# Optimization experiments

Hardware: AMD Instinct MI355X
Metric: run time of the kernel (lower is better)

The kernel has to match this reference:

```python
import jax, jax.numpy as jnp
import numpy as np

N, C, D, H = 4096, 64, 128, 4
CD = 2 * D          # combined_dim = 2*input_size
DQ = CD // 8        # per-head query/key dim


def _mlp(x, W1, b1, W2, b2):
    # MLP(in, hidden, out): Linear -> ReLU -> Linear
    return jax.nn.relu(x @ W1.T + b1) @ W2.T + b2


def _gru(x, h, Wih, bih, Whh, bhh):
    # torch.nn.GRUCell math
    gi = x @ Wih.T + bih
    gh = h @ Whh.T + bhh
    ir, iz, inn = jnp.split(gi, 3, axis=-1)
    hr, hz, hn = jnp.split(gh, 3, axis=-1)
    r = jax.nn.sigmoid(ir + hr)
    z = jax.nn.sigmoid(iz + hz)
    n = jnp.tanh(inn + r * hn)
    return (1.0 - z) * n + z * h


def setup_inputs() -> dict:
    key = jax.random.key(0)
    ks = jax.random.split(key, 16)
    def w(k, shape, fan):
        return jax.random.normal(k, shape, jnp.float32) / np.float32(np.sqrt(fan))
    return {
        "x": jax.random.normal(ks[0], (N, D), jnp.float32),
        "h": jax.random.normal(ks[1], (N, D), jnp.float32),
        "cluster_h": jax.random.normal(ks[2], (C, D), jnp.float32),
        "query_vectors": jax.random.normal(ks[3], (C, D), jnp.float32),
        "cluster_labels": jax.random.randint(ks[4], (N,), 0, C),
        "nodes_ind": jnp.arange(N),
        "edge_index_intra": jax.random.randint(ks[5], (2, 1024), 0, N),
        "num_clusters": C,
        "Wq": w(ks[6], (H, DQ, CD), CD), "bq": jnp.zeros((H, DQ), jnp.float32),
        "Wk": w(ks[7], (H, DQ, CD), CD), "bk": jnp.zeros((H, DQ), jnp.float32),
        "Wv": w(ks[8], (H, CD, CD), CD), "bv": jnp.zeros((H, CD), jnp.float32),
        "W1": w(ks[9], (CD, H * CD), H * CD), "b1": jnp.zeros((CD,), jnp.float32),
        "W2": w(ks[10], (CD, CD), CD), "b2": jnp.zeros((CD,), jnp.float32),
        "gru_Wih": w(ks[11], (3 * D, D), D), "gru_bih": jnp.zeros((3 * D,), jnp.float32),
        "gru_Whh": w(ks[12], (3 * D, D), D), "gru_bhh": jnp.zeros((3 * D,), jnp.float32),
        "Wp": 0.1 * w(ks[13], (D, D), D), "bp": jnp.zeros((D,), jnp.float32),
    }


def reference(x, h, cluster_h, query_vectors, cluster_labels, nodes_ind,
              edge_index_intra, num_clusters,
              Wq, bq, Wk, bk, Wv, bv, W1, b1, W2, b2,
              gru_Wih, gru_bih, gru_Whh, gru_bhh, Wp, bp):
    combined = jnp.concatenate([x, h], axis=-1)              # [N, 2D]
    # multi-head dense attention over all nodes (heads vectorized)
    q = jnp.einsum('nd,hed->hne', combined, Wq) + bq[:, None, :]   # [H,N,DQ]
    k = jnp.einsum('nd,hed->hne', combined, Wk) + bk[:, None, :]
    v = jnp.einsum('nd,hed->hne', combined, Wv) + bv[:, None, :]   # [H,N,2D]
    scores = jnp.einsum('hne,hme->hnm', q, k) / jnp.sqrt(jnp.float32(DQ))
    attn = jax.nn.softmax(jax.nn.leaky_relu(scores, 0.2), axis=-1)  # [H,N,N]
    hp = jnp.einsum('hnm,hme->hne', attn, v)                 # [H,N,2D]
    hp = jnp.transpose(hp, (1, 0, 2)).reshape(combined.shape[0], -1)  # [N,H*2D]
    node_repr = _mlp(hp, W1, b1, W2, b2) + combined          # [N,2D]
    # per-cluster mean of previous node hidden states
    ones = jnp.ones((h.shape[0],), h.dtype)
    counts = jax.ops.segment_sum(ones, cluster_labels, num_segments=num_clusters)
    sums = jax.ops.segment_sum(h, cluster_labels, num_segments=num_clusters)
    agg = sums / jnp.maximum(counts, 1.0)[:, None]           # [C,D]
    present = (counts > 0)[:, None]
    new_ch = _gru(agg, cluster_h, gru_Wih, gru_bih, gru_Whh, gru_bhh)
    updated_cluster_h = jnp.where(present, new_ch, cluster_h)  # [C,D]
    # cluster-to-node projection broadcast back to nodes
    c2n = (updated_cluster_h @ Wp.T + bp)[cluster_labels]    # [N,D]
    updated_h = node_repr[:, D:] + c2n                       # [N,D]
    return updated_h, updated_cluster_h
```

## Files before the change

### kernel.cpp

```cpp
#include <hip/hip_runtime.h>
#include <math.h>

#define N_NODES 4096
#define NHEADS  4
#define NSPLIT  4
#define KVRANGE 1024

typedef _Float16 f16;
typedef _Float16 half8 __attribute__((ext_vector_type(8)));
typedef float f32x4 __attribute__((ext_vector_type(4)));

template <int EPI>
__device__ __forceinline__ void gemm_body(const f16* __restrict__ A,
                                          const f16* __restrict__ B,
                                          const float* __restrict__ bias,
                                          const float* __restrict__ resid,
                                          const int* __restrict__ lab,
                                          const float* __restrict__ c2n,
                                          void* __restrict__ outv,
                                          int M, int K, int J, float alpha,
                                          int bx, int by, f16* smem) {
  f16* As = smem;
  f16* Bs = smem + 64 * 64;
  const int t  = threadIdx.x;
  const int mb = bx * 64, jb = by * 64;
  const int w  = t >> 6, l = t & 63;
  const int g_ = l >> 4, c_ = l & 15;
  const int m0 = (w >> 1) * 32, n0 = (w & 1) * 32;

  f32x4 acc[2][2];
#pragma unroll
  for (int i = 0; i < 2; ++i)
#pragma unroll
    for (int j = 0; j < 2; ++j) acc[i][j] = (f32x4){0.f, 0.f, 0.f, 0.f};

#define FRAG16(BUF, row, kh) \
  (*(const half8*)&BUF[(size_t)(row) * 64 + (((((kh) * 4 + g_) ^ (c_ & 7))) << 3)])

  for (int kb = 0; kb < K; kb += 64) {
    __syncthreads();
#pragma unroll
    for (int i = 0; i < 2; ++i) {
      int f = t + i * 256;
      int r = f >> 3, ch = f & 7;
      *(uint4*)&As[r * 64 + ((ch ^ (r & 7)) << 3)] =
          *(const uint4*)&A[(size_t)(mb + r) * K + kb + ch * 8];
      *(uint4*)&Bs[r * 64 + ((ch ^ (r & 7)) << 3)] =
          *(const uint4*)&B[(size_t)(jb + r) * K + kb + ch * 8];
    }
    __syncthreads();
#pragma unroll
    for (int kh = 0; kh < 2; ++kh) {
      half8 a0 = FRAG16(As, m0 + c_, kh);
      half8 a1 = FRAG16(As, m0 + 16 + c_, kh);
      half8 b0 = FRAG16(Bs, n0 + c_, kh);
      half8 b1 = FRAG16(Bs, n0 + 16 + c_, kh);
      acc[0][0] = __builtin_amdgcn_mfma_f32_16x16x32_f16(a0, b0, acc[0][0], 0, 0, 0);
      acc[0][1] = __builtin_amdgcn_mfma_f32_16x16x32_f16(a0, b1, acc[0][1], 0, 0, 0);
      acc[1][0] = __builtin_amdgcn_mfma_f32_16x16x32_f16(a1, b0, acc[1][0], 0, 0, 0);
      acc[1][1] = __builtin_amdgcn_mfma_f32_16x16x32_f16(a1, b1, acc[1][1], 0, 0, 0);
    }
  }
#undef FRAG16

#pragma unroll
  for (int mt = 0; mt < 2; ++mt)
#pragma unroll
    for (int nt = 0; nt < 2; ++nt) {
      int mbase = mb + m0 + mt * 16 + g_ * 4;
      int jj    = jb + n0 + nt * 16 + c_;
      if (EPI == 0 || EPI == 1) {
        f16* out = (f16*)outv;
        float bc = bias[jj];
#pragma unroll
        for (int r = 0; r < 4; ++r) {
          float v = (acc[mt][nt][r] + bc) * alpha;
          if (EPI == 1) v = fmaxf(v, 0.f);
          out[(size_t)(mbase + r) * J + jj] = (f16)v;
        }
      } else if (EPI == 2) {
        f16* out = (f16*)outv;
#pragma unroll
        for (int r = 0; r < 4; ++r)
          out[(size_t)(mbase + r) * J + jj] = (f16)(acc[mt][nt][r] + bias[mbase + r]);
      } else {
        float* out = (float*)outv;
        float bc = bias[jj];
#pragma unroll
        for (int r = 0; r < 4; ++r) {
          int m = mbase + r;
          out[(size_t)m * J + jj] = acc[mt][nt][r] + bc +
              resid[(size_t)m * J + jj] + c2n[lab[m] * 128 + jj];
        }
      }
    }
}

template <int EPI>
__global__ __launch_bounds__(256) void k_gemm16(const f16* __restrict__ A,
                                                const f16* __restrict__ B,
                                                const float* __restrict__ bias,
                                                const float* __restrict__ resid,
                                                const int* __restrict__ lab,
                                                const float* __restrict__ c2n,
                                                void* __restrict__ outv,
                                                int M, int K, int J, float alpha) {
  __shared__ f16 smem[2 * 64 * 64];
  gemm_body<EPI>(A, B, bias, resid, lab, c2n, outv, M, K, J, alpha,
                 blockIdx.x, blockIdx.y, smem);
}

__global__ __launch_bounds__(256) void k_prep(const float* __restrict__ x,
                                              const float* __restrict__ h,
                                              const float* __restrict__ Wq,
                                              const float* __restrict__ Wk,
                                              const float* __restrict__ Wv,
                                              const float* __restrict__ W1,
                                              const float* __restrict__ W2,
                                              f16* __restrict__ comb16,
                                              f16* __restrict__ pool,
                                              float* __restrict__ sums) {
  const int b = blockIdx.x, t = threadIdx.x;
  if (b < 1024) {
    int i = b * 256 + t;
    int n = i >> 6, c = i & 63;
    float4 v;
    if (c < 32) v = ((const float4*)x)[n * 32 + c];
    else        v = ((const float4*)h)[n * 32 + (c - 32)];
    union { uint2 u; f16 h4[4]; } pk;
    pk.h4[0] = (f16)v.x; pk.h4[1] = (f16)v.y; pk.h4[2] = (f16)v.z; pk.h4[3] = (f16)v.w;
    *(uint2*)&comb16[(size_t)i * 4] = pk.u;
  } else if (b < 1664) {
    int i4 = ((b - 1024) * 256 + t) * 4;
    const float* src; int off;
    if      (i4 <  32768) { src = Wq; off = 0; }
    else if (i4 <  65536) { src = Wk; off = 32768; }
    else if (i4 < 327680) { src = Wv; off = 65536; }
    else if (i4 < 589824) { src = W1; off = 327680; }
    else                  { src = W2; off = 589824; }
    float4 v = *(const float4*)&src[i4 - off];
    union { uint2 u; f16 h4[4]; } pk;
    pk.h4[0] = (f16)v.x; pk.h4[1] = (f16)v.y; pk.h4[2] = (f16)v.z; pk.h4[3] = (f16)v.w;
    *(uint2*)&pool[i4] = pk.u;
  } else {
    int i = (b - 1664) * 256 + t;
    if (i < 8256) sums[i] = 0.f;
  }
}

__global__ __launch_bounds__(256) void k_qkv(const f16* __restrict__ comb16,
                                             const f16* __restrict__ wq16,
                                             const f16* __restrict__ wk16,
                                             const f16* __restrict__ wv16,
                                             const float* __restrict__ bq,
                                             const float* __restrict__ bk,
                                             const float* __restrict__ bv,
                                             f16* __restrict__ qf16,
                                             f16* __restrict__ kf16,
                                             f16* __restrict__ vt16,
                                             const float* __restrict__ h,
                                             const int* __restrict__ lab,
                                             float* __restrict__ sums,
                                             float* __restrict__ cnt,
                                             float qscale) {
  __shared__ f16 smem[2 * 64 * 64];
  const int b = blockIdx.x;
  if (b < 1024) {
    gemm_body<2>(wv16, comb16, bv, nullptr, nullptr, nullptr, vt16,
                 1024, 256, 4096, 1.0f, b & 15, b >> 4, smem);
  } else if (b < 1152) {
    int r = b - 1024;
    gemm_body<0>(comb16, wq16, bq, nullptr, nullptr, nullptr, qf16,
                 4096, 256, 128, qscale, r & 63, r >> 6, smem);
  } else if (b < 1280) {
    int r = b - 1152;
    gemm_body<0>(comb16, wk16, bk, nullptr, nullptr, nullptr, kf16,
                 4096, 256, 128, 1.0f, r & 63, r >> 6, smem);
  } else {
    int i = (b - 1280) * 256 + threadIdx.x;
    int n = i >> 7, d = i & 127;
    int c = lab[n];
    atomicAdd(&sums[c * 128 + d], h[i]);
    if (d == 0) atomicAdd(&cnt[c], 1.0f);
  }
}

__global__ __launch_bounds__(256, 3) void k_attn_mfma(const f16* __restrict__ qg,
                                                      const f16* __restrict__ kg,
                                                      const f16* __restrict__ vt,
                                                      f16* __restrict__ pO,
                                                      float* __restrict__ pM,
                                                      float* __restrict__ pL) {
  const int hd  = blockIdx.y;
  const int sp  = blockIdx.z;
  const int kv0 = sp * KVRANGE;
  const int t   = threadIdx.x;
  const int w   = t >> 6, l = t & 63;
  const int g   = l >> 4, c = l & 15;
  const int qb  = blockIdx.x * 64;

  __shared__ f16 Ks[32 * 40];
  __shared__ f16 Vs[256 * 40];
  __shared__ f16 Ps[64 * 40];
  __shared__ float CfS[64];

  half8 qf = *(const half8*)&qg[(size_t)(qb + w * 16 + c) * 128 + hd * 32 + g * 8];

  f32x4 oacc[4][4];
#pragma unroll
  for (int i = 0; i < 4; ++i)
#pragma unroll
    for (int j = 0; j < 4; ++j) oacc[i][j] = (f32x4){0.f, 0.f, 0.f, 0.f};
  float m_run = -INFINITY, l_run = 0.f;
  const f32x4 zero4 = {0.f, 0.f, 0.f, 0.f};

  for (int kb = 0; kb < KVRANGE; kb += 32) {
    __syncthreads();
    if (t < 128) {
      int r = t >> 2, c8 = (t & 3) * 8;
      *(uint4*)&Ks[r * 40 + c8] =
          *(const uint4*)&kg[(size_t)(kv0 + kb + r) * 128 + hd * 32 + c8];
    }
#pragma unroll
    for (int i = 0; i < 4; ++i) {
      int cc = i * 256 + t, d = cc >> 2, c8 = (cc & 3) * 8;
      *(uint4*)&Vs[d * 40 + c8] =
          *(const uint4*)&vt[(size_t)(hd * 256 + d) * 4096 + kv0 + kb + c8];
    }
    __syncthreads();

    f32x4 s0 = __builtin_amdgcn_mfma_f32_16x16x32_f16(
        *(const half8*)&Ks[(c) * 40 + g * 8], qf, zero4, 0, 0, 0);
    f32x4 s1 = __builtin_amdgcn_mfma_f32_16x16x32_f16(
        *(const half8*)&Ks[(16 + c) * 40 + g * 8], qf, zero4, 0, 0, 0);

    float sv[8];
#pragma unroll
    for (int r = 0; r < 4; ++r) {
      float a = s0[r]; sv[r]     = a > 0.f ? a : 0.2f * a;
      float b = s1[r]; sv[4 + r] = b > 0.f ? b : 0.2f * b;
    }
    float mx = sv[0];
#pragma unroll
    for (int r = 1; r < 8; ++r) mx = fmaxf(mx, sv[r]);
    mx = fmaxf(mx, __shfl_xor(mx, 16));
    mx = fmaxf(mx, __shfl_xor(mx, 32));

    float cf = 1.f;
    if (!__all(mx <= m_run + 8.f)) {
      float m_new = fmaxf(m_run, mx);
      cf = __expf(m_run - m_new);
      m_run = m_new;
    }
    float p[8], ps = 0.f;
#pragma unroll
    for (int r = 0; r < 8; ++r) { p[r] = __expf(sv[r] - m_run); ps += p[r]; }
    ps += __shfl_xor(ps, 16);
    ps += __shfl_xor(ps, 32);
    l_run = l_run * cf + ps;

    if (g == 0) CfS[w * 16 + c] = cf;
    {
      union { unsigned u; f16 h2[2]; } z;
      uint2 lo, hi;
      z.h2[0] = (f16)p[0]; z.h2[1] = (f16)p[1]; lo.x = z.u;
      z.h2[0] = (f16)p[2]; z.h2[1] = (f16)p[3]; lo.y = z.u;
      z.h2[0] = (f16)p[4]; z.h2[1] = (f16)p[5]; hi.x = z.u;
      z.h2[0] = (f16)p[6]; z.h2[1] = (f16)p[7]; hi.y = z.u;
      *(uint2*)&Ps[(w * 16 + c) * 40 + g * 4]      = lo;
      *(uint2*)&Ps[(w * 16 + c) * 40 + 16 + g * 4] = hi;
    }
    __syncthreads();

#pragma unroll
    for (int qt = 0; qt < 4; ++qt) {
      float cfq = CfS[qt * 16 + c];
      if (!__all(cfq == 1.f)) {
#pragma unroll
        for (int i = 0; i < 4; ++i) {
          oacc[i][qt][0] *= cfq; oacc[i][qt][1] *= cfq;
          oacc[i][qt][2] *= cfq; oacc[i][qt][3] *= cfq;
        }
      }
    }
    half8 pfr[4];
#pragma unroll
    for (int qt = 0; qt < 4; ++qt)
      pfr[qt] = *(const half8*)&Ps[(qt * 16 + c) * 40 + g * 8];
#pragma unroll
    for (int i = 0; i < 4; ++i) {
      half8 vfr = *(const half8*)&Vs[((w * 4 + i) * 16 + c) * 40 + g * 8];
#pragma unroll
      for (int qt = 0; qt < 4; ++qt)
        oacc[i][qt] = __builtin_amdgcn_mfma_f32_16x16x32_f16(vfr, pfr[qt], oacc[i][qt], 0, 0, 0);
    }
  }

  __syncthreads();
  if (g == 0) CfS[w * 16 + c] = l_run;
  __syncthreads();
  float linv[4];
#pragma unroll
  for (int qt = 0; qt < 4; ++qt) linv[qt] = 1.f / CfS[qt * 16 + c];
#pragma unroll
  for (int i = 0; i < 4; ++i)
#pragma unroll
    for (int qt = 0; qt < 4; ++qt)
#pragma unroll
      for (int r = 0; r < 4; ++r) {
        int j = hd * 256 + (w * 4 + i) * 16 + g * 4 + r;
        pO[(size_t)(sp * 1024 + j) * 4096 + qb + qt * 16 + c] =
            (f16)(oacc[i][qt][r] * linv[qt]);
      }
  if (g == 0) {
    pM[(sp * 4 + hd) * 4096 + qb + w * 16 + c] = m_run;
    pL[(sp * 4 + hd) * 4096 + qb + w * 16 + c] = l_run;
  }
}

__global__ __launch_bounds__(256) void k_mergeplus(const f16* __restrict__ pO,
                                                   const float* __restrict__ pM,
                                                   const float* __restrict__ pL,
                                                   f16* __restrict__ hp,
                                                   const float* __restrict__ sums,
                                                   const float* __restrict__ cnt,
                                                   const float* __restrict__ ch,
                                                   const float* __restrict__ gWih,
                                                   const float* __restrict__ gbih,
                                                   const float* __restrict__ gWhh,
                                                   const float* __restrict__ gbhh,
                                                   const float* __restrict__ Wp,
                                                   const float* __restrict__ bp,
                                                   float* __restrict__ out_uch,
                                                   float* __restrict__ c2n) {
  const int b = blockIdx.x, t = threadIdx.x;
  if (b < 1024) {
    __shared__ float wm[NSPLIT][64], wl[NSPLIT][64];
    __shared__ float tile[64][65];
    const int q0 = (b & 63) * 64, jb = (b >> 6) * 64;
    const int h  = jb >> 8;

    if (t < 64) {
#pragma unroll
      for (int s = 0; s < NSPLIT; ++s) {
        wm[s][t] = pM[(s * 4 + h) * 4096 + q0 + t];
        wl[s][t] = pL[(s * 4 + h) * 4096 + q0 + t];
      }
    }
    __syncthreads();

    const int q8 = (t & 7) * 8;
#pragma unroll
    for (int it = 0; it < 2; ++it) {
      int jl = (t >> 3) + it * 32;
      float wgt[NSPLIT][8], inv[8];
#pragma unroll
      for (int q = 0; q < 8; ++q) {
        float M = wm[0][q8 + q];
#pragma unroll
        for (int s = 1; s < NSPLIT; ++s) M = fmaxf(M, wm[s][q8 + q]);
        float den = 0.f;
#pragma unroll
        for (int s = 0; s < NSPLIT; ++s) {
          float wv = wl[s][q8 + q] * __expf(wm[s][q8 + q] - M);
          wgt[s][q] = wv; den += wv;
        }
        inv[q] = 1.f / den;
      }
      float o[8] = {0.f};
#pragma unroll
      for (int s = 0; s < NSPLIT; ++s) {
        union { uint4 u; f16 h8[8]; } raw;
        raw.u = *(const uint4*)&pO[(size_t)(s * 1024 + jb + jl) * 4096 + q0 + q8];
#pragma unroll
        for (int q = 0; q < 8; ++q) o[q] += wgt[s][q] * (float)raw.h8[q];
      }
#pragma unroll
      for (int q = 0; q < 8; ++q) tile[q8 + q][jl] = o[q] * inv[q];
    }
    __syncthreads();

#pragma unroll
    for (int it = 0; it < 2; ++it) {
      int ql = (t >> 3) + it * 32, chk = t & 7;
      union { uint4 u; f16 h8[8]; } pk;
#pragma unroll
      for (int k = 0; k < 8; ++k) pk.h8[k] = (f16)tile[ql][chk * 8 + k];
      *(uint4*)&hp[(size_t)(q0 + ql) * 1024 + jb + chk * 8] = pk.u;
    }
  } else {
    __shared__ float ax[2][128], hx[2][128], ul[2][128];
    const int cc = t >> 7, d = t & 127;
    const int c  = (b - 1024) * 2 + cc;
    float count = cnt[c];
    ax[cc][d] = sums[c * 128 + d] / fmaxf(count, 1.0f);
    hx[cc][d] = ch[c * 128 + d];
    __syncthreads();
    float gi[3], gh[3];
#pragma unroll
    for (int g = 0; g < 3; ++g) {
      const float4* wi4 = (const float4*)&gWih[(size_t)(g * 128 + d) * 128];
      const float4* wh4 = (const float4*)&gWhh[(size_t)(g * 128 + d) * 128];
      float si = 0.f, sh = 0.f;
#pragma unroll 8
      for (int e = 0; e < 32; ++e) {
        float4 wv = wi4[e], hv = wh4[e];
        si = fmaf(ax[cc][e*4+0], wv.x, si); si = fmaf(ax[cc][e*4+1], wv.y, si);
        si = fmaf(ax[cc][e*4+2], wv.z, si); si = fmaf(ax[cc][e*4+3], wv.w, si);
        sh = fmaf(hx[cc][e*4+0], hv.x, sh); sh = fmaf(hx[cc][e*4+1], hv.y, sh);
        sh = fmaf(hx[cc][e*4+2], hv.z, sh); sh = fmaf(hx[cc][e*4+3], hv.w, sh);
      }
      gi[g] = si + gbih[g * 128 + d];
      gh[g] = sh + gbhh[g * 128 + d];
    }
    float r = 1.f / (1.f + expf(-(gi[0] + gh[0])));
    float z = 1.f / (1.f + expf(-(gi[1] + gh[1])));
    float nn = tanhf(gi[2] + r * gh[2]);
    float hv = hx[cc][d];
    float nh = (1.f - z) * nn + z * hv;
    float res = (count > 0.f) ? nh : hv;
    ul[cc][d] = res;
    out_uch[c * 128 + d] = res;
    __syncthreads();
    const float4* w4 = (const float4*)&Wp[(size_t)d * 128];
    float s = 0.f;
#pragma unroll 8
    for (int e = 0; e < 32; ++e) {
      float4 wv = w4[e];
      s = fmaf(ul[cc][e*4+0], wv.x, s); s = fmaf(ul[cc][e*4+1], wv.y, s);
      s = fmaf(ul[cc][e*4+2], wv.z, s); s = fmaf(ul[cc][e*4+3], wv.w, s);
    }
    c2n[c * 128 + d] = s + bp[d];
  }
}

extern "C" void kernel_launch(void* const* d_in, const int* in_sizes, int n_in,
                              void* d_out, int out_size, void* d_ws, size_t ws_size,
                              hipStream_t stream) {
  const float* x    = (const float*)d_in[0];
  const float* h    = (const float*)d_in[1];
  const float* ch   = (const float*)d_in[2];
  const int*   lab  = (const int*)d_in[4];
  const float* Wq   = (const float*)d_in[8];
  const float* bq   = (const float*)d_in[9];
  const float* Wk   = (const float*)d_in[10];
  const float* bk   = (const float*)d_in[11];
  const float* Wv   = (const float*)d_in[12];
  const float* bv   = (const float*)d_in[13];
  const float* W1   = (const float*)d_in[14];
  const float* b1   = (const float*)d_in[15];
  const float* W2   = (const float*)d_in[16];
  const float* b2   = (const float*)d_in[17];
  const float* gWih = (const float*)d_in[18];
  const float* gbih = (const float*)d_in[19];
  const float* gWhh = (const float*)d_in[20];
  const float* gbhh = (const float*)d_in[21];
  const float* Wp   = (const float*)d_in[22];
  const float* bp   = (const float*)d_in[23];

  float* outp    = (float*)d_out;
  float* out_uch = outp + 4096 * 128;

  f16* comb16 = (f16*)d_ws;
  f16* w16    = comb16 + 4096 * 256;
  f16* wq16   = w16;
  f16* wk16   = w16 + 32768;
  f16* wv16   = w16 + 65536;
  f16* w116   = w16 + 327680;
  f16* w216   = w16 + 589824;
  f16* qf16   = w16 + 655360;
  f16* kf16   = qf16 + 4096 * 128;
  f16* vt16   = kf16 + 4096 * 128;
  f16* pO     = vt16 + 1024 * 4096;
  f16* hp16   = pO + (size_t)NSPLIT * 1024 * 4096;
  f16* y116   = hp16 + (size_t)4096 * 1024;
  float* pM   = (float*)(y116 + 4096 * 256);
  float* pL   = pM + NSPLIT * 4 * 4096;
  float* sums = pL + NSPLIT * 4 * 4096;
  float* cnt  = sums + 64 * 128;
  float* c2n  = cnt + 64;

  const float qscale = 0.17677669529663687f;

  k_prep<<<1697, 256, 0, stream>>>(x, h, Wq, Wk, Wv, W1, W2, comb16, w16, sums);
  k_qkv<<<3328, 256, 0, stream>>>(comb16, wq16, wk16, wv16, bq, bk, bv,
                                  qf16, kf16, vt16, h, lab, sums, cnt, qscale);
  k_attn_mfma<<<dim3(64, NHEADS, NSPLIT), 256, 0, stream>>>(qf16, kf16, vt16, pO, pM, pL);
  k_mergeplus<<<1056, 256, 0, stream>>>(pO, pM, pL, hp16, sums, cnt, ch,
                                        gWih, gbih, gWhh, gbhh, Wp, bp, out_uch, c2n);
  k_gemm16<1><<<dim3(64, 4), 256, 0, stream>>>(hp16, w116, b1, nullptr, nullptr, nullptr,
                                               y116, 4096, 1024, 256, 1.0f);
  k_gemm16<3><<<dim3(64, 2), 256, 0, stream>>>(y116, w216 + 128 * 256, b2 + 128, h, lab, c2n,
                                               outp, 4096, 256, 128, 1.0f);
}
```

Measured before the change: 259.5 us.

## Load K/V fragments directly from global and remap attention blocks per XCD

The attention kernel stops staging K and V tiles through shared memory and instead has each lane load its MFMA fragments straight from global memory, which removes one barrier and the LDS round trip per KV step. The grid is flattened to 1D and remapped so that blocks sharing the same head/split land on the same XCD, improving L2 reuse of K/V. It also raises the occupancy hint to 4 blocks per CU and wraps the PV MFMA loop in s_setprio. The risk is redundant global loads, since every wave fetches the same K fragments and there are uncoalesced strided V reads.

```diff
diff --git a/kernel.cpp b/kernel.cpp
--- a/kernel.cpp
+++ b/kernel.cpp
@@ -185,26 +185,32 @@
   }
 }
 
-__global__ __launch_bounds__(256, 3) void k_attn_mfma(const f16* __restrict__ qg,
+__global__ __launch_bounds__(256, 4) void k_attn_mfma(const f16* __restrict__ qg,
                                                       const f16* __restrict__ kg,
                                                       const f16* __restrict__ vt,
                                                       f16* __restrict__ pO,
                                                       float* __restrict__ pM,
                                                       float* __restrict__ pL) {
-  const int hd  = blockIdx.y;
-  const int sp  = blockIdx.z;
-  const int kv0 = sp * KVRANGE;
-  const int t   = threadIdx.x;
-  const int w   = t >> 6, l = t & 63;
-  const int g   = l >> 4, c = l & 15;
-  const int qb  = blockIdx.x * 64;
-
-  __shared__ f16 Ks[32 * 40];
-  __shared__ f16 Vs[256 * 40];
+  const int b     = blockIdx.x;
+  const int xcd   = b & 7;
+  const int i_    = b >> 3;
+  const int combo = xcd * 2 + (i_ >> 6);
+  const int qblk  = i_ & 63;
+  const int hd    = combo >> 2, sp = combo & 3;
+  const int kv0   = sp * KVRANGE;
+  const int qb    = qblk * 64;
+
+  const int t = threadIdx.x;
+  const int w = t >> 6, l = t & 63;
+  const int g = l >> 4, c = l & 15;
+
   __shared__ f16 Ps[64 * 40];
   __shared__ float CfS[64];
 
   half8 qf = *(const half8*)&qg[(size_t)(qb + w * 16 + c) * 128 + hd * 32 + g * 8];
+
+  const f16* kbase = &kg[(size_t)(kv0)*128 + hd * 32 + g * 8];
+  const f16* vbase = &vt[(size_t)(hd * 256) * 4096 + kv0 + g * 8];
 
   f32x4 oacc[4][4];
 #pragma unroll
@@ -216,29 +222,22 @@
 
   for (int kb = 0; kb < KVRANGE; kb += 32) {
     __syncthreads();
-    if (t < 128) {
-      int r = t >> 2, c8 = (t & 3) * 8;
-      *(uint4*)&Ks[r * 40 + c8] =
-          *(const uint4*)&kg[(size_t)(kv0 + kb + r) * 128 + hd * 32 + c8];
-    }
-#pragma unroll
-    for (int i = 0; i < 4; ++i) {
-      int cc = i * 256 + t, d = cc >> 2, c8 = (cc & 3) * 8;
-      *(uint4*)&Vs[d * 40 + c8] =
-          *(const uint4*)&vt[(size_t)(hd * 256 + d) * 4096 + kv0 + kb + c8];
-    }
-    __syncthreads();
-
-    f32x4 s0 = __builtin_amdgcn_mfma_f32_16x16x32_f16(
-        *(const half8*)&Ks[(c) * 40 + g * 8], qf, zero4, 0, 0, 0);
-    f32x4 s1 = __builtin_amdgcn_mfma_f32_16x16x32_f16(
-        *(const half8*)&Ks[(16 + c) * 40 + g * 8], qf, zero4, 0, 0, 0);
+
+    half8 kf0 = *(const half8*)&kbase[(size_t)(kb + c) * 128];
+    half8 kf1 = *(const half8*)&kbase[(size_t)(kb + 16 + c) * 128];
+    half8 vfr[4];
+#pragma unroll
+    for (int i = 0; i < 4; ++i)
+      vfr[i] = *(const half8*)&vbase[(size_t)((w * 4 + i) * 16 + c) * 4096 + kb];
+
+    f32x4 s0 = __builtin_amdgcn_mfma_f32_16x16x32_f16(kf0, qf, zero4, 0, 0, 0);
+    f32x4 s1 = __builtin_amdgcn_mfma_f32_16x16x32_f16(kf1, qf, zero4, 0, 0, 0);
 
     float sv[8];
 #pragma unroll
     for (int r = 0; r < 4; ++r) {
       float a = s0[r]; sv[r]     = a > 0.f ? a : 0.2f * a;
-      float b = s1[r]; sv[4 + r] = b > 0.f ? b : 0.2f * b;
+      float b2 = s1[r]; sv[4 + r] = b2 > 0.f ? b2 : 0.2f * b2;
     }
     float mx = sv[0];
 #pragma unroll
@@ -287,13 +286,14 @@
 #pragma unroll
     for (int qt = 0; qt < 4; ++qt)
       pfr[qt] = *(const half8*)&Ps[(qt * 16 + c) * 40 + g * 8];
+    __builtin_amdgcn_s_setprio(1);
 #pragma unroll
     for (int i = 0; i < 4; ++i) {
-      half8 vfr = *(const half8*)&Vs[((w * 4 + i) * 16 + c) * 40 + g * 8];
 #pragma unroll
       for (int qt = 0; qt < 4; ++qt)
-        oacc[i][qt] = __builtin_amdgcn_mfma_f32_16x16x32_f16(vfr, pfr[qt], oacc[i][qt], 0, 0, 0);
-    }
+        oacc[i][qt] = __builtin_amdgcn_mfma_f32_16x16x32_f16(vfr[i], pfr[qt], oacc[i][qt], 0, 0, 0);
+    }
+    __builtin_amdgcn_s_setprio(0);
   }
 
   __syncthreads();
@@ -485,7 +485,7 @@
   k_prep<<<1697, 256, 0, stream>>>(x, h, Wq, Wk, Wv, W1, W2, comb16, w16, sums);
   k_qkv<<<3328, 256, 0, stream>>>(comb16, wq16, wk16, wv16, bq, bk, bv,
                                   qf16, kf16, vt16, h, lab, sums, cnt, qscale);
-  k_attn_mfma<<<dim3(64, NHEADS, NSPLIT), 256, 0, stream>>>(qf16, kf16, vt16, pO, pM, pL);
+  k_attn_mfma<<<1024, 256, 0, stream>>>(qf16, kf16, vt16, pO, pM, pL);
   k_mergeplus<<<1056, 256, 0, stream>>>(pO, pM, pL, hp16, sums, cnt, ch,
                                         gWih, gbih, gWhh, gbhh, Wp, bp, out_uch, c2n);
   k_gemm16<1><<<dim3(64, 4), 256, 0, stream>>>(hp16, w116, b1, nullptr, nullptr, nullptr,
```

Result: slower. 281.3 us (+8.4%).

## Prefetch GEMM tiles into registers and move cluster GRU into attention kernel

Applied to the files above, without the earlier changes.

The GEMM body now loads the next K-tile of A and B into registers after the barrier, so global loads overlap the MFMA work on the current shared-memory tile. The per-cluster GRU and projection work moves out of the merge kernel into 32 extra blocks of the attention grid, so it runs alongside the long attention blocks instead of sitting at the tail of the merge. This adds register pressure in the GEMM and shares LDS between two roles in the attention kernel.

```diff
diff --git a/kernel.cpp b/kernel.cpp
--- a/kernel.cpp
+++ b/kernel.cpp
@@ -27,28 +27,36 @@
   const int w  = t >> 6, l = t & 63;
   const int g_ = l >> 4, c_ = l & 15;
   const int m0 = (w >> 1) * 32, n0 = (w & 1) * 32;
+  const int r0 = t >> 3, ch0 = t & 7;
 
   f32x4 acc[2][2];
 #pragma unroll
   for (int i = 0; i < 2; ++i)
 #pragma unroll
     for (int j = 0; j < 2; ++j) acc[i][j] = (f32x4){0.f, 0.f, 0.f, 0.f};
+
+  uint4 ra0 = *(const uint4*)&A[(size_t)(mb + r0) * K + ch0 * 8];
+  uint4 ra1 = *(const uint4*)&A[(size_t)(mb + r0 + 32) * K + ch0 * 8];
+  uint4 rb0 = *(const uint4*)&B[(size_t)(jb + r0) * K + ch0 * 8];
+  uint4 rb1 = *(const uint4*)&B[(size_t)(jb + r0 + 32) * K + ch0 * 8];
+  const int sw = (ch0 ^ (r0 & 7)) << 3;
 
 #define FRAG16(BUF, row, kh) \
   (*(const half8*)&BUF[(size_t)(row) * 64 + (((((kh) * 4 + g_) ^ (c_ & 7))) << 3)])
 
   for (int kb = 0; kb < K; kb += 64) {
     __syncthreads();
-#pragma unroll
-    for (int i = 0; i < 2; ++i) {
-      int f = t + i * 256;
-      int r = f >> 3, ch = f & 7;
-      *(uint4*)&As[r * 64 + ((ch ^ (r & 7)) << 3)] =
-          *(const uint4*)&A[(size_t)(mb + r) * K + kb + ch * 8];
-      *(uint4*)&Bs[r * 64 + ((ch ^ (r & 7)) << 3)] =
-          *(const uint4*)&B[(size_t)(jb + r) * K + kb + ch * 8];
-    }
-    __syncthreads();
+    *(uint4*)&As[r0 * 64 + sw]        = ra0;
+    *(uint4*)&As[(r0 + 32) * 64 + sw] = ra1;
+    *(uint4*)&Bs[r0 * 64 + sw]        = rb0;
+    *(uint4*)&Bs[(r0 + 32) * 64 + sw] = rb1;
+    __syncthreads();
+    if (kb + 64 < K) {
+      ra0 = *(const uint4*)&A[(size_t)(mb + r0) * K + kb + 64 + ch0 * 8];
+      ra1 = *(const uint4*)&A[(size_t)(mb + r0 + 32) * K + kb + 64 + ch0 * 8];
+      rb0 = *(const uint4*)&B[(size_t)(jb + r0) * K + kb + 64 + ch0 * 8];
+      rb1 = *(const uint4*)&B[(size_t)(jb + r0 + 32) * K + kb + 64 + ch0 * 8];
+    }
 #pragma unroll
     for (int kh = 0; kh < 2; ++kh) {
       half8 a0 = FRAG16(As, m0 + c_, kh);
@@ -190,19 +198,80 @@
                                                       const f16* __restrict__ vt,
                                                       f16* __restrict__ pO,
                                                       float* __restrict__ pM,
-                                                      float* __restrict__ pL) {
-  const int hd  = blockIdx.y;
-  const int sp  = blockIdx.z;
-  const int kv0 = sp * KVRANGE;
-  const int t   = threadIdx.x;
-  const int w   = t >> 6, l = t & 63;
-  const int g   = l >> 4, c = l & 15;
-  const int qb  = blockIdx.x * 64;
-
+                                                      float* __restrict__ pL,
+                                                      const float* __restrict__ sums,
+                                                      const float* __restrict__ cnt,
+                                                      const float* __restrict__ ch,
+                                                      const float* __restrict__ gWih,
+                                                      const float* __restrict__ gbih,
+                                                      const float* __restrict__ gWhh,
+                                                      const float* __restrict__ gbhh,
+                                                      const float* __restrict__ Wp,
+                                                      const float* __restrict__ bp,
+                                                      float* __restrict__ out_uch,
+                                                      float* __restrict__ c2n) {
   __shared__ f16 Ks[32 * 40];
   __shared__ f16 Vs[256 * 40];
   __shared__ f16 Ps[64 * 40];
   __shared__ float CfS[64];
+
+  const int hd  = blockIdx.y;
+  const int sp  = blockIdx.z;
+  const int t   = threadIdx.x;
+
+  if (blockIdx.x >= 64) {
+    const int gid = (blockIdx.x - 64) * 16 + hd * 4 + sp;
+    float* ax = (float*)Vs;
+    float* hx = ax + 256;
+    float* ul = hx + 256;
+    const int cc = t >> 7, d = t & 127;
+    const int c  = gid * 2 + cc;
+    float count = cnt[c];
+    ax[cc * 128 + d] = sums[c * 128 + d] / fmaxf(count, 1.0f);
+    hx[cc * 128 + d] = ch[c * 128 + d];
+    __syncthreads();
+    float gi[3], gh[3];
+#pragma unroll
+    for (int g = 0; g < 3; ++g) {
+      const float4* wi4 = (const float4*)&gWih[(size_t)(g * 128 + d) * 128];
+      const float4* wh4 = (const float4*)&gWhh[(size_t)(g * 128 + d) * 128];
+      float si = 0.f, sh = 0.f;
+#pragma unroll 8
+      for (int e = 0; e < 32; ++e) {
+        float4 wv = wi4[e], hv = wh4[e];
+        si = fmaf(ax[cc*128+e*4+0], wv.x, si); si = fmaf(ax[cc*128+e*4+1], wv.y, si);
+        si = fmaf(ax[cc*128+e*4+2], wv.z, si); si = fmaf(ax[cc*128+e*4+3], wv.w, si);
+        sh = fmaf(hx[cc*128+e*4+0], hv.x, sh); sh = fmaf(hx[cc*128+e*4+1], hv.y, sh);
+        sh = fmaf(hx[cc*128+e*4+2], hv.z, sh); sh = fmaf(hx[cc*128+e*4+3], hv.w, sh);
+      }
+      gi[g] = si + gbih[g * 128 + d];
+      gh[g] = sh + gbhh[g * 128 + d];
+    }
+    float r = 1.f / (1.f + expf(-(gi[0] + gh[0])));
+    float z = 1.f / (1.f + expf(-(gi[1] + gh[1])));
+    float nn = tanhf(gi[2] + r * gh[2]);
+    float hv = hx[cc * 128 + d];
+    float nh = (1.f - z) * nn + z * hv;
+    float res = (count > 0.f) ? nh : hv;
+    ul[cc * 128 + d] = res;
+    out_uch[c * 128 + d] = res;
+    __syncthreads();
+    const float4* w4 = (const float4*)&Wp[(size_t)d * 128];
+    float s = 0.f;
+#pragma unroll 8
+    for (int e = 0; e < 32; ++e) {
+      float4 wv = w4[e];
+      s = fmaf(ul[cc*128+e*4+0], wv.x, s); s = fmaf(ul[cc*128+e*4+1], wv.y, s);
+      s = fmaf(ul[cc*128+e*4+2], wv.z, s); s = fmaf(ul[cc*128+e*4+3], wv.w, s);
+    }
+    c2n[c * 128 + d] = s + bp[d];
+    return;
+  }
+
+  const int kv0 = sp * KVRANGE;
+  const int w   = t >> 6, l = t & 63;
+  const int g   = l >> 4, c = l & 15;
+  const int qb  = blockIdx.x * 64;
 
   half8 qf = *(const half8*)&qg[(size_t)(qb + w * 16 + c) * 128 + hd * 32 + g * 8];
 
@@ -318,119 +387,63 @@
   }
 }
 
-__global__ __launch_bounds__(256) void k_mergeplus(const f16* __restrict__ pO,
-                                                   const float* __restrict__ pM,
-                                                   const float* __restrict__ pL,
-                                                   f16* __restrict__ hp,
-                                                   const float* __restrict__ sums,
-                                                   const float* __restrict__ cnt,
-                                                   const float* __restrict__ ch,
-                                                   const float* __restrict__ gWih,
-                                                   const float* __restrict__ gbih,
-                                                   const float* __restrict__ gWhh,
-                                                   const float* __restrict__ gbhh,
-                                                   const float* __restrict__ Wp,
-                                                   const float* __restrict__ bp,
-                                                   float* __restrict__ out_uch,
-                                                   float* __restrict__ c2n) {
+__global__ __launch_bounds__(256) void k_merge(const f16* __restrict__ pO,
+                                               const float* __restrict__ pM,
+                                               const float* __restrict__ pL,
+                                               f16* __restrict__ hp) {
   const int b = blockIdx.x, t = threadIdx.x;
-  if (b < 1024) {
-    __shared__ float wm[NSPLIT][64], wl[NSPLIT][64];
-    __shared__ float tile[64][65];
-    const int q0 = (b & 63) * 64, jb = (b >> 6) * 64;
-    const int h  = jb >> 8;
-
-    if (t < 64) {
+  __shared__ float wm[NSPLIT][64], wl[NSPLIT][64];
+  __shared__ float tile[64][65];
+  const int q0 = (b & 63) * 64, jb = (b >> 6) * 64;
+  const int h  = jb >> 8;
+
+  if (t < 64) {
+#pragma unroll
+    for (int s = 0; s < NSPLIT; ++s) {
+      wm[s][t] = pM[(s * 4 + h) * 4096 + q0 + t];
+      wl[s][t] = pL[(s * 4 + h) * 4096 + q0 + t];
+    }
+  }
+  __syncthreads();
+
+  const int q8 = (t & 7) * 8;
+#pragma unroll
+  for (int it = 0; it < 2; ++it) {
+    int jl = (t >> 3) + it * 32;
+    float wgt[NSPLIT][8], inv[8];
+#pragma unroll
+    for (int q = 0; q < 8; ++q) {
+      float M = wm[0][q8 + q];
+#pragma unroll
+      for (int s = 1; s < NSPLIT; ++s) M = fmaxf(M, wm[s][q8 + q]);
+      float den = 0.f;
 #pragma unroll
       for (int s = 0; s < NSPLIT; ++s) {
-        wm[s][t] = pM[(s * 4 + h) * 4096 + q0 + t];
-        wl[s][t] = pL[(s * 4 + h) * 4096 + q0 + t];
+        float wv = wl[s][q8 + q] * __expf(wm[s][q8 + q] - M);
+        wgt[s][q] = wv; den += wv;
       }
-    }
-    __syncthreads();
-
-    const int q8 = (t & 7) * 8;
-#pragma unroll
-    for (int it = 0; it < 2; ++it) {
-      int jl = (t >> 3) + it * 32;
-      float wgt[NSPLIT][8], inv[8];
-#pragma unroll
-      for (int q = 0; q < 8; ++q) {
-        float M = wm[0][q8 + q];
-#pragma unroll
-        for (int s = 1; s < NSPLIT; ++s) M = fmaxf(M, wm[s][q8 + q]);
-        float den = 0.f;
-#pragma unroll
-        for (int s = 0; s < NSPLIT; ++s) {
-          float wv = wl[s][q8 + q] * __expf(wm[s][q8 + q] - M);
-          wgt[s][q] = wv; den += wv;
-        }
-        inv[q] = 1.f / den;
-      }
-      float o[8] = {0.f};
-#pragma unroll
-      for (int s = 0; s < NSPLIT; ++s) {
-        union { uint4 u; f16 h8[8]; } raw;
-        raw.u = *(const uint4*)&pO[(size_t)(s * 1024 + jb + jl) * 4096 + q0 + q8];
-#pragma unroll
-        for (int q = 0; q < 8; ++q) o[q] += wgt[s][q] * (float)raw.h8[q];
-      }
-#pragma unroll
-      for (int q = 0; q < 8; ++q) tile[q8 + q][jl] = o[q] * inv[q];
-    }
-    __syncthreads();
-
-#pragma unroll
-    for (int it = 0; it < 2; ++it) {
-      int ql = (t >> 3) + it * 32, chk = t & 7;
-      union { uint4 u; f16 h8[8]; } pk;
-#pragma unroll
-      for (int k = 0; k < 8; ++k) pk.h8[k] = (f16)tile[ql][chk * 8 + k];
-      *(uint4*)&hp[(size_t)(q0 + ql) * 1024 + jb + chk * 8] = pk.u;
-    }
-  } else {
-    __shared__ float ax[2][128], hx[2][128], ul[2][128];
-    const int cc = t >> 7, d = t & 127;
-    const int c  = (b - 1024) * 2 + cc;
-    float count = cnt[c];
-    ax[cc][d] = sums[c * 128 + d] / fmaxf(count, 1.0f);
-    hx[cc][d] = ch[c * 128 + d];
-    __syncthreads();
-    float gi[3], gh[3];
-#pragma unroll
-    for (int g = 0; g < 3; ++g) {
-      const float4* wi4 = (const float4*)&gWih[(size_t)(g * 128 + d) * 128];
-      const float4* wh4 = (const float4*)&gWhh[(size_t)(g * 128 + d) * 128];
-      float si = 0.f, sh = 0.f;
-#pragma unroll 8
-      for (int e = 0; e < 32; ++e) {
-        float4 wv = wi4[e], hv = wh4[e];
-        si = fmaf(ax[cc][e*4+0], wv.x, si); si = fmaf(ax[cc][e*4+1], wv.y, si);
-        si = fmaf(ax[cc][e*4+2], wv.z, si); si = fmaf(ax[cc][e*4+3], wv.w, si);
-        sh = fmaf(hx[cc][e*4+0], hv.x, sh); sh = fmaf(hx[cc][e*4+1], hv.y, sh);
-        sh = fmaf(hx[cc][e*4+2], hv.z, sh); sh = fmaf(hx[cc][e*4+3], hv.w, sh);
-      }
-      gi[g] = si + gbih[g * 128 + d];
-      gh[g] = sh + gbhh[g * 128 + d];
-    }
-    float r = 1.f / (1.f + expf(-(gi[0] + gh[0])));
-    float z = 1.f / (1.f + expf(-(gi[1] + gh[1])));
-    float nn = tanhf(gi[2] + r * gh[2]);
-    float hv = hx[cc][d];
-    float nh = (1.f - z) * nn + z * hv;
-    float res = (count > 0.f) ? nh : hv;
-    ul[cc][d] = res;
-    out_uch[c * 128 + d] = res;
-    __syncthreads();
-    const float4* w4 = (const float4*)&Wp[(size_t)d * 128];
-    float s = 0.f;
-#pragma unroll 8
-    for (int e = 0; e < 32; ++e) {
-      float4 wv = w4[e];
-      s = fmaf(ul[cc][e*4+0], wv.x, s); s = fmaf(ul[cc][e*4+1], wv.y, s);
-      s = fmaf(ul[cc][e*4+2], wv.z, s); s = fmaf(ul[cc][e*4+3], wv.w, s);
-    }
-    c2n[c * 128 + d] = s + bp[d];
+      inv[q] = 1.f / den;
+    }
+    float o[8] = {0.f};
+#pragma unroll
+    for (int s = 0; s < NSPLIT; ++s) {
+      union { uint4 u; f16 h8[8]; } raw;
+      raw.u = *(const uint4*)&pO[(size_t)(s * 1024 + jb + jl) * 4096 + q0 + q8];
+#pragma unroll
+      for (int q = 0; q < 8; ++q) o[q] += wgt[s][q] * (float)raw.h8[q];
+    }
+#pragma unroll
+    for (int q = 0; q < 8; ++q) tile[q8 + q][jl] = o[q] * inv[q];
+  }
+  __syncthreads();
+
+#pragma unroll
+  for (int it = 0; it < 2; ++it) {
+    int ql = (t >> 3) + it * 32, chk = t & 7;
+    union { uint4 u; f16 h8[8]; } pk;
+#pragma unroll
+    for (int k = 0; k < 8; ++k) pk.h8[k] = (f16)tile[ql][chk * 8 + k];
+    *(uint4*)&hp[(size_t)(q0 + ql) * 1024 + jb + chk * 8] = pk.u;
   }
 }
 
@@ -485,9 +498,10 @@
   k_prep<<<1697, 256, 0, stream>>>(x, h, Wq, Wk, Wv, W1, W2, comb16, w16, sums);
   k_qkv<<<3328, 256, 0, stream>>>(comb16, wq16, wk16, wv16, bq, bk, bv,
                                   qf16, kf16, vt16, h, lab, sums, cnt, qscale);
-  k_attn_mfma<<<dim3(64, NHEADS, NSPLIT), 256, 0, stream>>>(qf16, kf16, vt16, pO, pM, pL);
-  k_mergeplus<<<1056, 256, 0, stream>>>(pO, pM, pL, hp16, sums, cnt, ch,
-                                        gWih, gbih, gWhh, gbhh, Wp, bp, out_uch, c2n);
+  k_attn_mfma<<<dim3(66, NHEADS, NSPLIT), 256, 0, stream>>>(
+      qf16, kf16, vt16, pO, pM, pL,
+      sums, cnt, ch, gWih, gbih, gWhh, gbhh, Wp, bp, out_uch, c2n);
+  k_merge<<<1024, 256, 0, stream>>>(pO, pM, pL, hp16);
   k_gemm16<1><<<dim3(64, 4), 256, 0, stream>>>(hp16, w116, b1, nullptr, nullptr, nullptr,
                                                y116, 4096, 1024, 256, 1.0f);
   k_gemm16<3><<<dim3(64, 2), 256, 0, stream>>>(y116, w216 + 128 * 256, b2 + 128, h, lab, c2n,
```

Result: faster. 253.6 us (-2.3%).

## Register-prefetch GEMM tiles and remap attention blocks for XCD-local K/V reuse

Applied to the files above, without the earlier changes.

The shared GEMM body now loads the next K-tile of A and B into registers while the current tile is consumed by MFMA, so global load latency overlaps compute. The loop keeps one barrier per iteration before the MFMAs; the barrier at the top of the loop still protects the LDS rewrite. The attention kernel switches to a 1D grid of 1024 blocks and remaps block IDs so that each XCD (block index mod 8) handles two fixed head/split combinations. Blocks reading the same K/V range then share that XCD's L2. The trade-off is more live registers in the GEMM and dependence on round-robin XCD dispatch.

```diff
diff --git a/kernel.cpp b/kernel.cpp
--- a/kernel.cpp
+++ b/kernel.cpp
@@ -27,28 +27,36 @@
   const int w  = t >> 6, l = t & 63;
   const int g_ = l >> 4, c_ = l & 15;
   const int m0 = (w >> 1) * 32, n0 = (w & 1) * 32;
+  const int r0 = t >> 3, ch0 = t & 7;
 
   f32x4 acc[2][2];
 #pragma unroll
   for (int i = 0; i < 2; ++i)
 #pragma unroll
     for (int j = 0; j < 2; ++j) acc[i][j] = (f32x4){0.f, 0.f, 0.f, 0.f};
+
+  uint4 ra0 = *(const uint4*)&A[(size_t)(mb + r0) * K + ch0 * 8];
+  uint4 ra1 = *(const uint4*)&A[(size_t)(mb + r0 + 32) * K + ch0 * 8];
+  uint4 rb0 = *(const uint4*)&B[(size_t)(jb + r0) * K + ch0 * 8];
+  uint4 rb1 = *(const uint4*)&B[(size_t)(jb + r0 + 32) * K + ch0 * 8];
+  const int sw = (ch0 ^ (r0 & 7)) << 3;
 
 #define FRAG16(BUF, row, kh) \
   (*(const half8*)&BUF[(size_t)(row) * 64 + (((((kh) * 4 + g_) ^ (c_ & 7))) << 3)])
 
   for (int kb = 0; kb < K; kb += 64) {
     __syncthreads();
-#pragma unroll
-    for (int i = 0; i < 2; ++i) {
-      int f = t + i * 256;
-      int r = f >> 3, ch = f & 7;
-      *(uint4*)&As[r * 64 + ((ch ^ (r & 7)) << 3)] =
-          *(const uint4*)&A[(size_t)(mb + r) * K + kb + ch * 8];
-      *(uint4*)&Bs[r * 64 + ((ch ^ (r & 7)) << 3)] =
-          *(const uint4*)&B[(size_t)(jb + r) * K + kb + ch * 8];
-    }
-    __syncthreads();
+    *(uint4*)&As[r0 * 64 + sw]        = ra0;
+    *(uint4*)&As[(r0 + 32) * 64 + sw] = ra1;
+    *(uint4*)&Bs[r0 * 64 + sw]        = rb0;
+    *(uint4*)&Bs[(r0 + 32) * 64 + sw] = rb1;
+    __syncthreads();
+    if (kb + 64 < K) {
+      ra0 = *(const uint4*)&A[(size_t)(mb + r0) * K + kb + 64 + ch0 * 8];
+      ra1 = *(const uint4*)&A[(size_t)(mb + r0 + 32) * K + kb + 64 + ch0 * 8];
+      rb0 = *(const uint4*)&B[(size_t)(jb + r0) * K + kb + 64 + ch0 * 8];
+      rb1 = *(const uint4*)&B[(size_t)(jb + r0 + 32) * K + kb + 64 + ch0 * 8];
+    }
 #pragma unroll
     for (int kh = 0; kh < 2; ++kh) {
       half8 a0 = FRAG16(As, m0 + c_, kh);
@@ -191,13 +199,18 @@
                                                       f16* __restrict__ pO,
                                                       float* __restrict__ pM,
                                                       float* __restrict__ pL) {
-  const int hd  = blockIdx.y;
-  const int sp  = blockIdx.z;
-  const int kv0 = sp * KVRANGE;
-  const int t   = threadIdx.x;
-  const int w   = t >> 6, l = t & 63;
-  const int g   = l >> 4, c = l & 15;
-  const int qb  = blockIdx.x * 64;
+  const int b     = blockIdx.x;
+  const int xcd   = b & 7;
+  const int i_    = b >> 3;
+  const int combo = xcd * 2 + (i_ >> 6);
+  const int qblk  = i_ & 63;
+  const int hd    = combo >> 2, sp = combo & 3;
+  const int kv0   = sp * KVRANGE;
+  const int qb    = qblk * 64;
+
+  const int t = threadIdx.x;
+  const int w = t >> 6, l = t & 63;
+  const int g = l >> 4, c = l & 15;
 
   __shared__ f16 Ks[32 * 40];
   __shared__ f16 Vs[256 * 40];
@@ -238,7 +251,7 @@
 #pragma unroll
     for (int r = 0; r < 4; ++r) {
       float a = s0[r]; sv[r]     = a > 0.f ? a : 0.2f * a;
-      float b = s1[r]; sv[4 + r] = b > 0.f ? b : 0.2f * b;
+      float b2 = s1[r]; sv[4 + r] = b2 > 0.f ? b2 : 0.2f * b2;
     }
     float mx = sv[0];
 #pragma unroll
@@ -485,7 +498,7 @@
   k_prep<<<1697, 256, 0, stream>>>(x, h, Wq, Wk, Wv, W1, W2, comb16, w16, sums);
   k_qkv<<<3328, 256, 0, stream>>>(comb16, wq16, wk16, wv16, bq, bk, bv,
                                   qf16, kf16, vt16, h, lab, sums, cnt, qscale);
-  k_attn_mfma<<<dim3(64, NHEADS, NSPLIT), 256, 0, stream>>>(qf16, kf16, vt16, pO, pM, pL);
+  k_attn_mfma<<<1024, 256, 0, stream>>>(qf16, kf16, vt16, pO, pM, pL);
   k_mergeplus<<<1056, 256, 0, stream>>>(pO, pM, pL, hp16, sums, cnt, ch,
                                         gWih, gbih, gWhh, gbhh, Wp, bp, out_uch, c2n);
   k_gemm16<1><<<dim3(64, 4), 256, 0, stream>>>(hp16, w116, b1, nullptr, nullptr, nullptr,
```

Result: faster. 253.5 us (-2.3%).
